# Kernel tuning notes

Hardware: AMD Instinct MI355X
Metric: run time of the kernel (lower is better)

Reference implementation:

```python
import jax, jax.numpy as jnp
import numpy as np
from jax import lax


def setup_inputs() -> dict:
    key = jax.random.key(0)
    k1, k2 = jax.random.split(key)
    B, H, W, C = 8, 32, 32, 512
    N = 16384
    feature_batch = jax.random.normal(k1, (B, H, W, C), dtype=jnp.float32)
    mb = jax.random.normal(k2, (N, C), dtype=jnp.float32)
    return {"feature_batch": feature_batch, "mb": mb, "b": 9}


def reference(feature_batch, mb, b):
    B, H, W, C = feature_batch.shape
    fv = feature_batch.reshape(B * H * W, C)                       # (Q, C)
    sq = (
        jnp.sum(fv * fv, axis=1)[:, None]
        + jnp.sum(mb * mb, axis=1)[None, :]
        - 2.0 * (fv @ mb.T)
    )                                                               # (Q, N)
    sq = jnp.maximum(sq, 0.0)  # guard fp round-off before sqrt
    # smallest-b distances, sorted ascending (top_k of negated values)
    neg_topk = lax.top_k(-sq, b)[0]                                 # (Q, b)
    top_k_dists_squared = -neg_topk
    pixel_scores = jnp.sqrt(top_k_dists_squared[:, 0]).reshape(B, H * W)
    max_idx = jnp.argmax(pixel_scores, axis=1)                      # (B,)
    softmax_args = jnp.sqrt(
        top_k_dists_squared.reshape(B, H * W, b)[jnp.arange(B), max_idx, :]
    )                                                               # (B, b)
    image_scores = softmax_args[:, 0]
    if b > 1:
        image_scores = image_scores * (1.0 - jax.nn.softmax(softmax_args, axis=1)[:, 0])
    pixel_scores = pixel_scores.reshape(B, 1, H, W)
    return pixel_scores, image_scores
```

## Files before the change

### kernel.cpp

```cpp
#include <hip/hip_runtime.h>
#include <hip/hip_bf16.h>

typedef unsigned short u16;

#define M_ROWS 8192
#define N_ROWS 16384
#define KDIM   512
#define BM     128
#define BN     128
#define BK     64
#define NCHUNKS 8
#define NPER   (N_ROWS / NCHUNKS)
#define TOPK   9

typedef __attribute__((ext_vector_type(8)))  short bf16x8;
typedef __attribute__((ext_vector_type(16))) float f32x16;

__device__ __forceinline__ void gload_lds16(const void* g, void* l) {
  __builtin_amdgcn_global_load_lds(
      (const __attribute__((address_space(1))) void*)g,
      (__attribute__((address_space(3))) void*)l,
      16, 0, 0);
}

__device__ __forceinline__ u16 f2bf(float x) {
  union { float f; unsigned u; } c; c.f = x;
  unsigned u = c.u;
  u += 0x7fffu + ((u >> 16) & 1u);
  return (u16)(u >> 16);
}

__device__ __forceinline__ void topk_update(float v, float best[TOPK]) {
  if (v < best[TOPK - 1]) {
    #pragma unroll
    for (int i = 0; i < TOPK; ++i) {
      float b = best[i];
      best[i] = fminf(b, v);
      v = fmaxf(b, v);
    }
  }
}

__global__ __launch_bounds__(256) void prep_kernel(
    const float* __restrict__ fv, const float* __restrict__ mb,
    u16* __restrict__ fvb, u16* __restrict__ mbb,
    float* __restrict__ nf, float* __restrict__ nm_perm)
{
  int idx = blockIdx.x * 4 + (threadIdx.x >> 6);
  int l = threadIdx.x & 63;
  const float* src; u16* dst;
  if (idx < M_ROWS) {
    src = fv + (size_t)idx * KDIM; dst = fvb + (size_t)idx * KDIM;
  } else {
    int r = idx - M_ROWS;
    src = mb + (size_t)r * KDIM; dst = mbb + (size_t)r * KDIM;
  }
  float4 x0 = ((const float4*)src)[2 * l];
  float4 x1 = ((const float4*)src)[2 * l + 1];
  float s = x0.x * x0.x + x0.y * x0.y + x0.z * x0.z + x0.w * x0.w
          + x1.x * x1.x + x1.y * x1.y + x1.z * x1.z + x1.w * x1.w;
  uint4 o;
  o.x = (unsigned)f2bf(x0.x) | ((unsigned)f2bf(x0.y) << 16);
  o.y = (unsigned)f2bf(x0.z) | ((unsigned)f2bf(x0.w) << 16);
  o.z = (unsigned)f2bf(x1.x) | ((unsigned)f2bf(x1.y) << 16);
  o.w = (unsigned)f2bf(x1.z) | ((unsigned)f2bf(x1.w) << 16);
  ((uint4*)dst)[l] = o;
  #pragma unroll
  for (int off = 32; off > 0; off >>= 1) s += __shfl_down(s, off, 64);
  if (l == 0) {
    if (idx < M_ROWS) {
      nf[idx] = s;
    } else {
      int n  = idx - M_ROWS;
      int ig = n >> 5;
      int w5 = n & 31;
      int h  = (w5 >> 2) & 1;
      int r  = (w5 & 3) | ((w5 >> 3) << 2);
      nm_perm[(ig * 2 + h) * 16 + r] = s;
    }
  }
}

__global__ __launch_bounds__(256) void gemm_topk_kernel(
    const u16* __restrict__ fvb, const u16* __restrict__ mbb,
    const float* __restrict__ nm_perm, float* __restrict__ partial)
{
  __shared__ __align__(16) u16 As[BM * BK];
  __shared__ __align__(16) u16 Bs[BN * BK];

  const int t   = threadIdx.x;
  const int l   = t & 63;
  const int w   = t >> 6;
  const int h   = l >> 5;
  const int c31 = l & 31;
  const int cx  = c31 & 7;

  const int m0    = blockIdx.x * BM;
  const int ncoff = blockIdx.y * NPER;

  const int srow_lo = l >> 3;
  const int sc      = ((l & 7) ^ srow_lo) * 8;

  float best[TOPK];
  #pragma unroll
  for (int i = 0; i < TOPK; ++i) best[i] = 3.4e38f;
  float T = 3.4e38f;

  for (int nt = 0; nt < NPER / BN; ++nt) {
    const int nbase = ncoff + nt * BN;
    f32x16 acc[4];
    #pragma unroll
    for (int i = 0; i < 4; ++i)
      #pragma unroll
      for (int r = 0; r < 16; ++r) acc[i][r] = 0.0f;

    for (int kc = 0; kc < KDIM / BK; ++kc) {
      __syncthreads();
      const int kb = kc * BK + sc;
      #pragma unroll
      for (int i = 0; i < 4; ++i) {
        gload_lds16(fvb + (size_t)(m0 + w * 32 + i * 8 + srow_lo) * KDIM + kb,
                    &As[(w * 32 + i * 8) * BK]);
        gload_lds16(mbb + (size_t)(nbase + w * 32 + i * 8 + srow_lo) * KDIM + kb,
                    &Bs[(w * 32 + i * 8) * BK]);
      }
      __syncthreads();
      #pragma unroll
      for (int kk = 0; kk < 4; ++kk) {
        const int ch = ((kk * 2 + h) ^ cx) * 8;
        bf16x8 fvf = *(const bf16x8*)&As[(w * 32 + c31) * BK + ch];
        #pragma unroll
        for (int i = 0; i < 4; ++i) {
          bf16x8 mbf = *(const bf16x8*)&Bs[(i * 32 + c31) * BK + ch];
          acc[i] = __builtin_amdgcn_mfma_f32_32x32x16_bf16(mbf, fvf, acc[i], 0, 0, 0);
        }
      }
    }

    #pragma unroll
    for (int i = 0; i < 4; ++i) {
      const float4* np = (const float4*)&nm_perm[(((nbase >> 5) + i) * 2 + h) * 16];
      float v[16];
      float bmin = 3.4e38f;
      #pragma unroll
      for (int rr = 0; rr < 4; ++rr) {
        float4 q = np[rr];
        v[rr * 4 + 0] = fmaf(-2.0f, acc[i][rr * 4 + 0], q.x);
        v[rr * 4 + 1] = fmaf(-2.0f, acc[i][rr * 4 + 1], q.y);
        v[rr * 4 + 2] = fmaf(-2.0f, acc[i][rr * 4 + 2], q.z);
        v[rr * 4 + 3] = fmaf(-2.0f, acc[i][rr * 4 + 3], q.w);
      }
      #pragma unroll
      for (int r = 0; r < 16; ++r) bmin = fminf(bmin, v[r]);
      if (bmin < T) {
        #pragma unroll
        for (int r = 0; r < 16; ++r) topk_update(v[r], best);
      }
    }
    T = fminf(best[TOPK - 1], __shfl_xor(best[TOPK - 1], 32, 64));
  }

  {
    float tmp[TOPK];
    #pragma unroll
    for (int s = 0; s < TOPK; ++s) tmp[s] = __shfl_xor(best[s], 32, 64);
    #pragma unroll
    for (int s = 0; s < TOPK; ++s) topk_update(tmp[s], best);
  }
  int m = m0 + w * 32 + c31;
  size_t base = ((size_t)blockIdx.y * M_ROWS + m) * TOPK;
  if (h == 0) {
    #pragma unroll
    for (int s = 0; s < 5; ++s) partial[base + s] = best[s];
  } else {
    #pragma unroll
    for (int s = 5; s < TOPK; ++s) partial[base + s] = best[s];
  }
}

__global__ __launch_bounds__(256) void merge_kernel(
    const float* __restrict__ partial, const float* __restrict__ nf,
    float* __restrict__ final9, float* __restrict__ out_pix)
{
  int row = blockIdx.x * 256 + threadIdx.x;
  float best[TOPK];
  #pragma unroll
  for (int i = 0; i < TOPK; ++i) best[i] = 3.4e38f;
  for (int s = 0; s < NCHUNKS; ++s) {
    const float* p = &partial[((size_t)s * M_ROWS + row) * TOPK];
    #pragma unroll
    for (int i = 0; i < TOPK; ++i) topk_update(p[i], best);
  }
  float nfr = nf[row];
  float d[TOPK];
  #pragma unroll
  for (int i = 0; i < TOPK; ++i) d[i] = sqrtf(fmaxf(best[i] + nfr, 0.0f));
  out_pix[row] = d[0];
  #pragma unroll
  for (int i = 0; i < TOPK; ++i) final9[(size_t)row * TOPK + i] = d[i];
}

__global__ __launch_bounds__(256) void img_kernel(
    const float* __restrict__ out_pix, const float* __restrict__ final9,
    const int* __restrict__ bptr, float* __restrict__ out_img)
{
  int img = blockIdx.x, t = threadIdx.x;
  float bv = -1.0f; int bi = 0;
  for (int p = t; p < 1024; p += 256) {
    float v = out_pix[img * 1024 + p];
    if (v > bv) { bv = v; bi = p; }
  }
  __shared__ float sv[256];
  __shared__ int   si[256];
  sv[t] = bv; si[t] = bi;
  __syncthreads();
  for (int off = 128; off > 0; off >>= 1) {
    if (t < off) {
      float v2 = sv[t + off]; int i2 = si[t + off];
      if (v2 > sv[t] || (v2 == sv[t] && i2 < si[t])) { sv[t] = v2; si[t] = i2; }
    }
    __syncthreads();
  }
  if (t == 0) {
    int row = img * 1024 + si[0];
    int b = bptr[0];
    float s0 = final9[(size_t)row * TOPK + 0];
    float score = s0;
    if (b > 1) {
      int bb = b < TOPK ? b : TOPK;
      float mx = s0;
      for (int i = 1; i < bb; ++i) mx = fmaxf(mx, final9[(size_t)row * TOPK + i]);
      float den = 0.0f;
      for (int i = 0; i < bb; ++i) den += expf(final9[(size_t)row * TOPK + i] - mx);
      score = s0 * (1.0f - expf(s0 - mx) / den);
    }
    out_img[img] = score;
  }
}

extern "C" void kernel_launch(void* const* d_in, const int* in_sizes, int n_in,
                              void* d_out, int out_size, void* d_ws, size_t ws_size,
                              hipStream_t stream) {
  const float* fv   = (const float*)d_in[0];
  const float* mb   = (const float*)d_in[1];
  const int*   bptr = (const int*)d_in[2];
  float* out = (float*)d_out;

  char* w = (char*)d_ws;
  u16*   fvb     = (u16*)w;
  u16*   mbb     = (u16*)(w + 8388608);
  float* nf      = (float*)(w + 25165824);
  float* nm_perm = (float*)(w + 25198592);
  float* partial = (float*)(w + 25264128);
  float* final9  = (float*)(w + 27623424);

  hipLaunchKernelGGL(prep_kernel, dim3((M_ROWS + N_ROWS) / 4), dim3(256), 0, stream,
                     fv, mb, fvb, mbb, nf, nm_perm);
  hipLaunchKernelGGL(gemm_topk_kernel, dim3(M_ROWS / BM, NCHUNKS), dim3(256), 0, stream,
                     fvb, mbb, nm_perm, partial);
  hipLaunchKernelGGL(merge_kernel, dim3(M_ROWS / 256), dim3(256), 0, stream,
                     partial, nf, final9, out);
  hipLaunchKernelGGL(img_kernel, dim3(8), dim3(256), 0, stream,
                     out, final9, bptr, out + M_ROWS);
}
```

Baseline: 315.0 us.

## Rewrite GEMM-topk with 256x256 tiles, 4-stage LDS pipeline and 16x16 MFMA

```diff
diff --git a/kernel.cpp b/kernel.cpp
--- a/kernel.cpp
+++ b/kernel.cpp
@@ -1,25 +1,27 @@
 #include <hip/hip_runtime.h>
-#include <hip/hip_bf16.h>
 
 typedef unsigned short u16;
 
 #define M_ROWS 8192
 #define N_ROWS 16384
 #define KDIM   512
-#define BM     128
-#define BN     128
-#define BK     64
 #define NCHUNKS 8
 #define NPER   (N_ROWS / NCHUNKS)
 #define TOPK   9
 
-typedef __attribute__((ext_vector_type(8)))  short bf16x8;
-typedef __attribute__((ext_vector_type(16))) float f32x16;
-
-__device__ __forceinline__ void gload_lds16(const void* g, void* l) {
+#define BNT 256
+#define BMT 256
+#define BKT 32
+#define NT  (NPER / BNT)
+#define KT  (KDIM / BKT)
+
+typedef __attribute__((ext_vector_type(8))) short bf16x8;
+typedef __attribute__((ext_vector_type(4))) float f32x4;
+
+__device__ __forceinline__ void gload_lds16(const void* gp, void* lp) {
   __builtin_amdgcn_global_load_lds(
-      (const __attribute__((address_space(1))) void*)g,
-      (__attribute__((address_space(3))) void*)l,
+      (const __attribute__((address_space(1))) void*)gp,
+      (__attribute__((address_space(3))) void*)lp,
       16, 0, 0);
 }
 
@@ -30,7 +32,7 @@
   return (u16)(u >> 16);
 }
 
-__device__ __forceinline__ void topk_update(float v, float best[TOPK]) {
+__device__ __forceinline__ void topk_update(float v, float* best) {
   if (v < best[TOPK - 1]) {
     #pragma unroll
     for (int i = 0; i < TOPK; ++i) {
@@ -44,7 +46,7 @@
 __global__ __launch_bounds__(256) void prep_kernel(
     const float* __restrict__ fv, const float* __restrict__ mb,
     u16* __restrict__ fvb, u16* __restrict__ mbb,
-    float* __restrict__ nf, float* __restrict__ nm_perm)
+    float* __restrict__ nf, float* __restrict__ nm)
 {
   int idx = blockIdx.x * 4 + (threadIdx.x >> 6);
   int l = threadIdx.x & 63;
@@ -68,113 +70,190 @@
   #pragma unroll
   for (int off = 32; off > 0; off >>= 1) s += __shfl_down(s, off, 64);
   if (l == 0) {
-    if (idx < M_ROWS) {
-      nf[idx] = s;
-    } else {
-      int n  = idx - M_ROWS;
-      int ig = n >> 5;
-      int w5 = n & 31;
-      int h  = (w5 >> 2) & 1;
-      int r  = (w5 & 3) | ((w5 >> 3) << 2);
-      nm_perm[(ig * 2 + h) * 16 + r] = s;
-    }
-  }
-}
-
-__global__ __launch_bounds__(256) void gemm_topk_kernel(
+    if (idx < M_ROWS) nf[idx] = s;
+    else              nm[idx - M_ROWS] = s;
+  }
+}
+
+#define MFMA_ROW(AF, NF)                                                          \
+  acc[NF][0] = __builtin_amdgcn_mfma_f32_16x16x32_bf16(AF, b0, acc[NF][0], 0, 0, 0); \
+  acc[NF][1] = __builtin_amdgcn_mfma_f32_16x16x32_bf16(AF, b1, acc[NF][1], 0, 0, 0); \
+  acc[NF][2] = __builtin_amdgcn_mfma_f32_16x16x32_bf16(AF, b2, acc[NF][2], 0, 0, 0); \
+  acc[NF][3] = __builtin_amdgcn_mfma_f32_16x16x32_bf16(AF, b3, acc[NF][3], 0, 0, 0);
+
+__global__ __launch_bounds__(512, 2) void gemm_topk_kernel(
     const u16* __restrict__ fvb, const u16* __restrict__ mbb,
-    const float* __restrict__ nm_perm, float* __restrict__ partial)
+    const float* __restrict__ nm, float* __restrict__ partial)
 {
-  __shared__ __align__(16) u16 As[BM * BK];
-  __shared__ __align__(16) u16 Bs[BN * BK];
+  extern __shared__ __align__(16) char smem[];
+  u16* const Ab = (u16*)smem;
+  u16* const Bb = (u16*)(smem + 65536);
+  float* const smerge = (float*)(smem + 131072);
 
   const int t   = threadIdx.x;
   const int l   = t & 63;
   const int w   = t >> 6;
-  const int h   = l >> 5;
-  const int c31 = l & 31;
-  const int cx  = c31 & 7;
-
-  const int m0    = blockIdx.x * BM;
+  const int wr  = w >> 2;
+  const int wc  = w & 3;
+  const int r16 = l & 15;
+  const int g   = l >> 4;
+
+  const int m0    = blockIdx.x * BMT;
   const int ncoff = blockIdx.y * NPER;
 
-  const int srow_lo = l >> 3;
-  const int sc      = ((l & 7) ^ srow_lo) * 8;
-
-  float best[TOPK];
-  #pragma unroll
-  for (int i = 0; i < TOPK; ++i) best[i] = 3.4e38f;
-  float T = 3.4e38f;
-
-  for (int nt = 0; nt < NPER / BN; ++nt) {
-    const int nbase = ncoff + nt * BN;
-    f32x16 acc[4];
-    #pragma unroll
-    for (int i = 0; i < 4; ++i)
+  const int sr4 = l >> 2;
+  const int sc4 = ((l & 3) ^ (sr4 & 3)) * 8;
+  const int ch  = (g ^ (r16 & 3)) * 8;
+  const int aoff = (wr * 128 + r16) * BKT + ch;
+  const int boff = (wc * 64 + r16) * BKT + ch;
+
+  float best[4][TOPK];
+  float T[4];
+  #pragma unroll
+  for (int mf = 0; mf < 4; ++mf) {
+    T[mf] = 3.4e38f;
+    #pragma unroll
+    for (int s = 0; s < TOPK; ++s) best[mf][s] = 3.4e38f;
+  }
+
+#define STAGE_A(nb, kt_, buf_) do {                                           \
+    _Pragma("unroll")                                                         \
+    for (int j_ = 0; j_ < 2; ++j_)                                            \
+      gload_lds16(mbb + (size_t)((nb) + j_ * 128 + w * 16 + sr4) * KDIM       \
+                      + (kt_) * BKT + sc4,                                    \
+                  Ab + (buf_) * 8192 + (j_ * 128 + w * 16) * BKT);            \
+  } while (0)
+#define STAGE_B(kt_, buf_) do {                                               \
+    _Pragma("unroll")                                                         \
+    for (int j_ = 0; j_ < 2; ++j_)                                            \
+      gload_lds16(fvb + (size_t)(m0 + j_ * 128 + w * 16 + sr4) * KDIM         \
+                      + (kt_) * BKT + sc4,                                    \
+                  Bb + (buf_) * 8192 + (j_ * 128 + w * 16) * BKT);            \
+  } while (0)
+
+  STAGE_A(ncoff, 0, 0); STAGE_B(0, 0);
+  STAGE_A(ncoff, 1, 1); STAGE_B(1, 1);
+  STAGE_A(ncoff, 2, 2); STAGE_B(2, 2);
+  asm volatile("s_waitcnt vmcnt(8)" ::: "memory");
+  __builtin_amdgcn_s_barrier();
+
+  for (int nt = 0; nt < NT; ++nt) {
+    const int nbase = ncoff + nt * BNT;
+    f32x4 acc[8][4];
+    #pragma unroll
+    for (int nf = 0; nf < 8; ++nf)
       #pragma unroll
-      for (int r = 0; r < 16; ++r) acc[i][r] = 0.0f;
-
-    for (int kc = 0; kc < KDIM / BK; ++kc) {
-      __syncthreads();
-      const int kb = kc * BK + sc;
+      for (int mf = 0; mf < 4; ++mf)
+        acc[nf][mf] = (f32x4){0.f, 0.f, 0.f, 0.f};
+
+    #pragma unroll
+    for (int kt = 0; kt < KT; ++kt) {
+      const u16* Ak = Ab + (kt & 3) * 8192;
+      const u16* Bk = Bb + (kt & 3) * 8192;
+
+      bf16x8 b0 = *(const bf16x8*)&Bk[boff +    0];
+      bf16x8 b1 = *(const bf16x8*)&Bk[boff +  512];
+      bf16x8 b2 = *(const bf16x8*)&Bk[boff + 1024];
+      bf16x8 b3 = *(const bf16x8*)&Bk[boff + 1536];
+      bf16x8 a0 = *(const bf16x8*)&Ak[aoff +    0];
+      bf16x8 a1 = *(const bf16x8*)&Ak[aoff +  512];
+      bf16x8 a2 = *(const bf16x8*)&Ak[aoff + 1024];
+      bf16x8 a3 = *(const bf16x8*)&Ak[aoff + 1536];
+      if (kt < KT - 3) {
+        STAGE_A(nbase, kt + 3, (kt + 3) & 3);
+      } else if (nt < NT - 1) {
+        STAGE_A(nbase + BNT, kt + 3 - KT, (kt + 3) & 3);
+      }
+      __builtin_amdgcn_s_barrier();
+      asm volatile("s_waitcnt lgkmcnt(0)" ::: "memory");
+      __builtin_amdgcn_s_setprio(1);
+      MFMA_ROW(a0, 0) MFMA_ROW(a1, 1) MFMA_ROW(a2, 2) MFMA_ROW(a3, 3)
+      __builtin_amdgcn_s_setprio(0);
+      __builtin_amdgcn_s_barrier();
+
+      bf16x8 a4 = *(const bf16x8*)&Ak[aoff + 2048];
+      bf16x8 a5 = *(const bf16x8*)&Ak[aoff + 2560];
+      bf16x8 a6 = *(const bf16x8*)&Ak[aoff + 3072];
+      bf16x8 a7 = *(const bf16x8*)&Ak[aoff + 3584];
+      if (kt < KT - 3) {
+        STAGE_B(kt + 3, (kt + 3) & 3);
+      } else if (nt < NT - 1) {
+        STAGE_B(kt + 3 - KT, (kt + 3) & 3);
+      }
+      __builtin_amdgcn_s_barrier();
+      asm volatile("s_waitcnt lgkmcnt(0)" ::: "memory");
+      __builtin_amdgcn_s_setprio(1);
+      MFMA_ROW(a4, 4) MFMA_ROW(a5, 5) MFMA_ROW(a6, 6) MFMA_ROW(a7, 7)
+      __builtin_amdgcn_s_setprio(0);
+      if (kt < KT - 3) {
+        asm volatile("s_waitcnt vmcnt(8)" ::: "memory");
+      } else if (kt == KT - 3) {
+        if (nt < NT - 1) { asm volatile("s_waitcnt vmcnt(8)" ::: "memory"); }
+        else             { asm volatile("s_waitcnt vmcnt(4)" ::: "memory"); }
+      } else {
+        if (nt < NT - 1) { asm volatile("s_waitcnt vmcnt(8)" ::: "memory"); }
+        else             { asm volatile("s_waitcnt vmcnt(0)" ::: "memory"); }
+      }
+      __builtin_amdgcn_s_barrier();
+    }
+
+    const float* nmp = nm + nbase + wr * 128 + g * 4;
+    #pragma unroll
+    for (int nf = 0; nf < 8; ++nf) {
+      const float4 q = *(const float4*)(nmp + nf * 16);
       #pragma unroll
-      for (int i = 0; i < 4; ++i) {
-        gload_lds16(fvb + (size_t)(m0 + w * 32 + i * 8 + srow_lo) * KDIM + kb,
-                    &As[(w * 32 + i * 8) * BK]);
-        gload_lds16(mbb + (size_t)(nbase + w * 32 + i * 8 + srow_lo) * KDIM + kb,
-                    &Bs[(w * 32 + i * 8) * BK]);
-      }
-      __syncthreads();
-      #pragma unroll
-      for (int kk = 0; kk < 4; ++kk) {
-        const int ch = ((kk * 2 + h) ^ cx) * 8;
-        bf16x8 fvf = *(const bf16x8*)&As[(w * 32 + c31) * BK + ch];
-        #pragma unroll
-        for (int i = 0; i < 4; ++i) {
-          bf16x8 mbf = *(const bf16x8*)&Bs[(i * 32 + c31) * BK + ch];
-          acc[i] = __builtin_amdgcn_mfma_f32_32x32x16_bf16(mbf, fvf, acc[i], 0, 0, 0);
+      for (int mf = 0; mf < 4; ++mf) {
+        float v0 = fmaf(-2.0f, acc[nf][mf][0], q.x);
+        float v1 = fmaf(-2.0f, acc[nf][mf][1], q.y);
+        float v2 = fmaf(-2.0f, acc[nf][mf][2], q.z);
+        float v3 = fmaf(-2.0f, acc[nf][mf][3], q.w);
+        float bm = fminf(fminf(v0, v1), fminf(v2, v3));
+        if (bm < T[mf]) {
+          topk_update(v0, best[mf]);
+          topk_update(v1, best[mf]);
+          topk_update(v2, best[mf]);
+          topk_update(v3, best[mf]);
+          T[mf] = best[mf][TOPK - 1];
         }
       }
     }
-
-    #pragma unroll
-    for (int i = 0; i < 4; ++i) {
-      const float4* np = (const float4*)&nm_perm[(((nbase >> 5) + i) * 2 + h) * 16];
-      float v[16];
-      float bmin = 3.4e38f;
+  }
+
+  #pragma unroll
+  for (int mf = 0; mf < 4; ++mf) {
+    float tmp[TOPK];
+    #pragma unroll
+    for (int s = 0; s < TOPK; ++s) tmp[s] = __shfl_xor(best[mf][s], 16, 64);
+    #pragma unroll
+    for (int s = 0; s < TOPK; ++s) topk_update(tmp[s], best[mf]);
+    #pragma unroll
+    for (int s = 0; s < TOPK; ++s) tmp[s] = __shfl_xor(best[mf][s], 32, 64);
+    #pragma unroll
+    for (int s = 0; s < TOPK; ++s) topk_update(tmp[s], best[mf]);
+  }
+
+  __syncthreads();
+  if (wr == 1 && g == 0) {
+    #pragma unroll
+    for (int mf = 0; mf < 4; ++mf)
       #pragma unroll
-      for (int rr = 0; rr < 4; ++rr) {
-        float4 q = np[rr];
-        v[rr * 4 + 0] = fmaf(-2.0f, acc[i][rr * 4 + 0], q.x);
-        v[rr * 4 + 1] = fmaf(-2.0f, acc[i][rr * 4 + 1], q.y);
-        v[rr * 4 + 2] = fmaf(-2.0f, acc[i][rr * 4 + 2], q.z);
-        v[rr * 4 + 3] = fmaf(-2.0f, acc[i][rr * 4 + 3], q.w);
-      }
+      for (int s = 0; s < TOPK; ++s)
+        smerge[(wc * 64 + mf * 16 + r16) * TOPK + s] = best[mf][s];
+  }
+  __syncthreads();
+  if (wr == 0) {
+    #pragma unroll
+    for (int mf = 0; mf < 4; ++mf) {
+      const float* p = &smerge[(wc * 64 + mf * 16 + r16) * TOPK];
       #pragma unroll
-      for (int r = 0; r < 16; ++r) bmin = fminf(bmin, v[r]);
-      if (bmin < T) {
-        #pragma unroll
-        for (int r = 0; r < 16; ++r) topk_update(v[r], best);
-      }
-    }
-    T = fminf(best[TOPK - 1], __shfl_xor(best[TOPK - 1], 32, 64));
-  }
-
-  {
-    float tmp[TOPK];
-    #pragma unroll
-    for (int s = 0; s < TOPK; ++s) tmp[s] = __shfl_xor(best[s], 32, 64);
-    #pragma unroll
-    for (int s = 0; s < TOPK; ++s) topk_update(tmp[s], best);
-  }
-  int m = m0 + w * 32 + c31;
-  size_t base = ((size_t)blockIdx.y * M_ROWS + m) * TOPK;
-  if (h == 0) {
-    #pragma unroll
-    for (int s = 0; s < 5; ++s) partial[base + s] = best[s];
-  } else {
-    #pragma unroll
-    for (int s = 5; s < TOPK; ++s) partial[base + s] = best[s];
+      for (int s = 0; s < TOPK; ++s) topk_update(p[s], best[mf]);
+      const int m = m0 + wc * 64 + mf * 16 + r16;
+      float* dst = &partial[((size_t)blockIdx.y * M_ROWS + m) * TOPK];
+      if (g == 0)      { dst[0] = best[mf][0]; dst[1] = best[mf][1]; dst[2] = best[mf][2]; }
+      else if (g == 1) { dst[3] = best[mf][3]; dst[4] = best[mf][4]; }
+      else if (g == 2) { dst[5] = best[mf][5]; dst[6] = best[mf][6]; }
+      else             { dst[7] = best[mf][7]; dst[8] = best[mf][8]; }
+    }
   }
 }
 
@@ -246,18 +325,18 @@
   const int*   bptr = (const int*)d_in[2];
   float* out = (float*)d_out;
 
-  char* w = (char*)d_ws;
-  u16*   fvb     = (u16*)w;
-  u16*   mbb     = (u16*)(w + 8388608);
-  float* nf      = (float*)(w + 25165824);
-  float* nm_perm = (float*)(w + 25198592);
-  float* partial = (float*)(w + 25264128);
-  float* final9  = (float*)(w + 27623424);
+  char* ws = (char*)d_ws;
+  u16*   fvb     = (u16*)ws;
+  u16*   mbb     = (u16*)(ws + 8388608);
+  float* nf      = (float*)(ws + 25165824);
+  float* nm      = (float*)(ws + 25198592);
+  float* partial = (float*)(ws + 25264128);
+  float* final9  = (float*)(ws + 27623424);
 
   hipLaunchKernelGGL(prep_kernel, dim3((M_ROWS + N_ROWS) / 4), dim3(256), 0, stream,
-                     fv, mb, fvb, mbb, nf, nm_perm);
-  hipLaunchKernelGGL(gemm_topk_kernel, dim3(M_ROWS / BM, NCHUNKS), dim3(256), 0, stream,
-                     fvb, mbb, nm_perm, partial);
+                     fv, mb, fvb, mbb, nf, nm);
+  hipLaunchKernelGGL(gemm_topk_kernel, dim3(M_ROWS / BMT, NCHUNKS), dim3(512),
+                     140288, stream, fvb, mbb, nm, partial);
   hipLaunchKernelGGL(merge_kernel, dim3(M_ROWS / 256), dim3(256), 0, stream,
                      partial, nf, final9, out);
   hipLaunchKernelGGL(img_kernel, dim3(8), dim3(256), 0, stream,
```

New measurement: 426.8 us. 35.5% more time.

## Double per-warp M tile to reuse B fragments and split N into more chunks

Applied to the files above, without the earlier changes.

```diff
diff --git a/kernel.cpp b/kernel.cpp
--- a/kernel.cpp
+++ b/kernel.cpp
@@ -1,15 +1,14 @@
 #include <hip/hip_runtime.h>
-#include <hip/hip_bf16.h>
 
 typedef unsigned short u16;
 
 #define M_ROWS 8192
 #define N_ROWS 16384
 #define KDIM   512
-#define BM     128
+#define BM     256
 #define BN     128
 #define BK     64
-#define NCHUNKS 8
+#define NCHUNKS 16
 #define NPER   (N_ROWS / NCHUNKS)
 #define TOPK   9
 
@@ -30,7 +29,7 @@
   return (u16)(u >> 16);
 }
 
-__device__ __forceinline__ void topk_update(float v, float best[TOPK]) {
+__device__ __forceinline__ void topk_update(float v, float* best) {
   if (v < best[TOPK - 1]) {
     #pragma unroll
     for (int i = 0; i < TOPK; ++i) {
@@ -81,7 +80,7 @@
   }
 }
 
-__global__ __launch_bounds__(256) void gemm_topk_kernel(
+__global__ __launch_bounds__(256, 2) void gemm_topk_kernel(
     const u16* __restrict__ fvb, const u16* __restrict__ mbb,
     const float* __restrict__ nm_perm, float* __restrict__ partial)
 {
@@ -101,38 +100,47 @@
   const int srow_lo = l >> 3;
   const int sc      = ((l & 7) ^ srow_lo) * 8;
 
-  float best[TOPK];
-  #pragma unroll
-  for (int i = 0; i < TOPK; ++i) best[i] = 3.4e38f;
-  float T = 3.4e38f;
+  float best[2][TOPK];
+  float T[2];
+  #pragma unroll
+  for (int s = 0; s < 2; ++s) {
+    T[s] = 3.4e38f;
+    #pragma unroll
+    for (int i = 0; i < TOPK; ++i) best[s][i] = 3.4e38f;
+  }
 
   for (int nt = 0; nt < NPER / BN; ++nt) {
     const int nbase = ncoff + nt * BN;
-    f32x16 acc[4];
-    #pragma unroll
-    for (int i = 0; i < 4; ++i)
-      #pragma unroll
-      for (int r = 0; r < 16; ++r) acc[i][r] = 0.0f;
+    f32x16 acc[2][4];
+    #pragma unroll
+    for (int s = 0; s < 2; ++s)
+      #pragma unroll
+      for (int i = 0; i < 4; ++i)
+        #pragma unroll
+        for (int r = 0; r < 16; ++r) acc[s][i][r] = 0.0f;
 
     for (int kc = 0; kc < KDIM / BK; ++kc) {
       __syncthreads();
       const int kb = kc * BK + sc;
       #pragma unroll
-      for (int i = 0; i < 4; ++i) {
-        gload_lds16(fvb + (size_t)(m0 + w * 32 + i * 8 + srow_lo) * KDIM + kb,
-                    &As[(w * 32 + i * 8) * BK]);
+      for (int i = 0; i < 8; ++i)
+        gload_lds16(fvb + (size_t)(m0 + w * 64 + i * 8 + srow_lo) * KDIM + kb,
+                    &As[(w * 64 + i * 8) * BK]);
+      #pragma unroll
+      for (int i = 0; i < 4; ++i)
         gload_lds16(mbb + (size_t)(nbase + w * 32 + i * 8 + srow_lo) * KDIM + kb,
                     &Bs[(w * 32 + i * 8) * BK]);
-      }
       __syncthreads();
       #pragma unroll
       for (int kk = 0; kk < 4; ++kk) {
         const int ch = ((kk * 2 + h) ^ cx) * 8;
-        bf16x8 fvf = *(const bf16x8*)&As[(w * 32 + c31) * BK + ch];
+        bf16x8 f0 = *(const bf16x8*)&As[(w * 64 +      c31) * BK + ch];
+        bf16x8 f1 = *(const bf16x8*)&As[(w * 64 + 32 + c31) * BK + ch];
         #pragma unroll
         for (int i = 0; i < 4; ++i) {
           bf16x8 mbf = *(const bf16x8*)&Bs[(i * 32 + c31) * BK + ch];
-          acc[i] = __builtin_amdgcn_mfma_f32_32x32x16_bf16(mbf, fvf, acc[i], 0, 0, 0);
+          acc[0][i] = __builtin_amdgcn_mfma_f32_32x32x16_bf16(mbf, f0, acc[0][i], 0, 0, 0);
+          acc[1][i] = __builtin_amdgcn_mfma_f32_32x32x16_bf16(mbf, f1, acc[1][i], 0, 0, 0);
         }
       }
     }
@@ -140,41 +148,57 @@
     #pragma unroll
     for (int i = 0; i < 4; ++i) {
       const float4* np = (const float4*)&nm_perm[(((nbase >> 5) + i) * 2 + h) * 16];
-      float v[16];
-      float bmin = 3.4e38f;
-      #pragma unroll
-      for (int rr = 0; rr < 4; ++rr) {
-        float4 q = np[rr];
-        v[rr * 4 + 0] = fmaf(-2.0f, acc[i][rr * 4 + 0], q.x);
-        v[rr * 4 + 1] = fmaf(-2.0f, acc[i][rr * 4 + 1], q.y);
-        v[rr * 4 + 2] = fmaf(-2.0f, acc[i][rr * 4 + 2], q.z);
-        v[rr * 4 + 3] = fmaf(-2.0f, acc[i][rr * 4 + 3], q.w);
+      float4 q0 = np[0], q1 = np[1], q2 = np[2], q3 = np[3];
+      #pragma unroll
+      for (int s = 0; s < 2; ++s) {
+        float v[16];
+        v[ 0] = fmaf(-2.0f, acc[s][i][ 0], q0.x);
+        v[ 1] = fmaf(-2.0f, acc[s][i][ 1], q0.y);
+        v[ 2] = fmaf(-2.0f, acc[s][i][ 2], q0.z);
+        v[ 3] = fmaf(-2.0f, acc[s][i][ 3], q0.w);
+        v[ 4] = fmaf(-2.0f, acc[s][i][ 4], q1.x);
+        v[ 5] = fmaf(-2.0f, acc[s][i][ 5], q1.y);
+        v[ 6] = fmaf(-2.0f, acc[s][i][ 6], q1.z);
+        v[ 7] = fmaf(-2.0f, acc[s][i][ 7], q1.w);
+        v[ 8] = fmaf(-2.0f, acc[s][i][ 8], q2.x);
+        v[ 9] = fmaf(-2.0f, acc[s][i][ 9], q2.y);
+        v[10] = fmaf(-2.0f, acc[s][i][10], q2.z);
+        v[11] = fmaf(-2.0f, acc[s][i][11], q2.w);
+        v[12] = fmaf(-2.0f, acc[s][i][12], q3.x);
+        v[13] = fmaf(-2.0f, acc[s][i][13], q3.y);
+        v[14] = fmaf(-2.0f, acc[s][i][14], q3.z);
+        v[15] = fmaf(-2.0f, acc[s][i][15], q3.w);
+        float bmin = 3.4e38f;
+        #pragma unroll
+        for (int r = 0; r < 16; ++r) bmin = fminf(bmin, v[r]);
+        if (bmin < T[s]) {
+          #pragma unroll
+          for (int r = 0; r < 16; ++r) topk_update(v[r], best[s]);
+          T[s] = best[s][TOPK - 1];
+        }
       }
-      #pragma unroll
-      for (int r = 0; r < 16; ++r) bmin = fminf(bmin, v[r]);
-      if (bmin < T) {
-        #pragma unroll
-        for (int r = 0; r < 16; ++r) topk_update(v[r], best);
-      }
-    }
-    T = fminf(best[TOPK - 1], __shfl_xor(best[TOPK - 1], 32, 64));
-  }
-
-  {
+    }
+    #pragma unroll
+    for (int s = 0; s < 2; ++s)
+      T[s] = fminf(best[s][TOPK - 1], __shfl_xor(best[s][TOPK - 1], 32, 64));
+  }
+
+  #pragma unroll
+  for (int s = 0; s < 2; ++s) {
     float tmp[TOPK];
     #pragma unroll
-    for (int s = 0; s < TOPK; ++s) tmp[s] = __shfl_xor(best[s], 32, 64);
-    #pragma unroll
-    for (int s = 0; s < TOPK; ++s) topk_update(tmp[s], best);
-  }
-  int m = m0 + w * 32 + c31;
-  size_t base = ((size_t)blockIdx.y * M_ROWS + m) * TOPK;
-  if (h == 0) {
-    #pragma unroll
-    for (int s = 0; s < 5; ++s) partial[base + s] = best[s];
-  } else {
-    #pragma unroll
-    for (int s = 5; s < TOPK; ++s) partial[base + s] = best[s];
+    for (int q = 0; q < TOPK; ++q) tmp[q] = __shfl_xor(best[s][q], 32, 64);
+    #pragma unroll
+    for (int q = 0; q < TOPK; ++q) topk_update(tmp[q], best[s]);
+    int m = m0 + w * 64 + s * 32 + c31;
+    size_t base = ((size_t)blockIdx.y * M_ROWS + m) * TOPK;
+    if (h == 0) {
+      #pragma unroll
+      for (int q = 0; q < 5; ++q) partial[base + q] = best[s][q];
+    } else {
+      #pragma unroll
+      for (int q = 5; q < TOPK; ++q) partial[base + q] = best[s][q];
+    }
   }
 }
 
@@ -246,13 +270,13 @@
   const int*   bptr = (const int*)d_in[2];
   float* out = (float*)d_out;
 
-  char* w = (char*)d_ws;
-  u16*   fvb     = (u16*)w;
-  u16*   mbb     = (u16*)(w + 8388608);
-  float* nf      = (float*)(w + 25165824);
-  float* nm_perm = (float*)(w + 25198592);
-  float* partial = (float*)(w + 25264128);
-  float* final9  = (float*)(w + 27623424);
+  char* ws = (char*)d_ws;
+  u16*   fvb     = (u16*)ws;
+  u16*   mbb     = (u16*)(ws + 8388608);
+  float* nf      = (float*)(ws + 25165824);
+  float* nm_perm = (float*)(ws + 25198592);
+  float* partial = (float*)(ws + 25264128);
+  float* final9  = (float*)(ws + 29982720);
 
   hipLaunchKernelGGL(prep_kernel, dim3((M_ROWS + N_ROWS) / 4), dim3(256), 0, stream,
                      fv, mb, fvb, mbb, nf, nm_perm);
```

Result: no change. 310.1 us (-1.6%).
